# Kernel optimization log

Hardware: AMD Instinct MI355X
Metric: run time of the kernel (lower is better)

## Reference

```python
import jax, jax.numpy as jnp
import numpy as np

DIM = 1024
HEADS = 16
HEAD_DIM = DIM // HEADS
EXPANSION = 4
HIDDEN = int(DIM * EXPANSION * 2 / 3)  # 2730, per FFN code
LS_INIT = 1e-5
EPS = 1e-6


def setup_inputs() -> dict:
    key = jax.random.key(0)
    ks = jax.random.split(key, 16)
    s = lambda fan_in: 1.0 / np.sqrt(fan_in)
    return {
        "x": jax.random.normal(ks[0], (4, 1024, DIM), dtype=jnp.float32),
        "mask": jnp.ones((4, 1, 1, 1024), dtype=bool),
        "ln1_g": jnp.ones((DIM,), jnp.float32),
        "ln1_b": jnp.zeros((DIM,), jnp.float32),
        "qkv_w": jax.random.normal(ks[1], (DIM, 3 * DIM), jnp.float32) * s(DIM),
        "qkv_b": jnp.zeros((3 * DIM,), jnp.float32),
        "inter": jax.random.normal(ks[2], (HEADS, HEAD_DIM, HEAD_DIM), jnp.float32) * s(HEAD_DIM),
        "pl_w": jax.random.normal(ks[3], (HEADS, HEADS), jnp.float32) * s(HEADS),
        "pl_b": jnp.zeros((HEADS,), jnp.float32),
        "pw_w": jax.random.normal(ks[4], (HEADS, HEADS), jnp.float32) * s(HEADS),
        "pw_b": jnp.zeros((HEADS,), jnp.float32),
        "proj_w": jax.random.normal(ks[5], (DIM, DIM), jnp.float32) * s(DIM),
        "proj_b": jnp.zeros((DIM,), jnp.float32),
        "gamma1": jnp.full((DIM,), LS_INIT, jnp.float32),
        "ln2_g": jnp.ones((DIM,), jnp.float32),
        "ln2_b": jnp.zeros((DIM,), jnp.float32),
        "w_wide": jax.random.normal(ks[6], (DIM, HIDDEN), jnp.float32) * s(DIM),
        "w_gate": jax.random.normal(ks[7], (DIM, HIDDEN), jnp.float32) * s(DIM),
        "w_out": jax.random.normal(ks[8], (HIDDEN, DIM), jnp.float32) * s(HIDDEN),
        "gamma2": jnp.full((DIM,), LS_INIT, jnp.float32),
    }


def _layernorm(x, g, b):
    mu = jnp.mean(x, axis=-1, keepdims=True)
    var = jnp.mean(jnp.square(x - mu), axis=-1, keepdims=True)
    return (x - mu) * jax.lax.rsqrt(var + EPS) * g + b


def _forward(x, mask, ln1_g, ln1_b, qkv_w, qkv_b, inter, pl_w, pl_b, pw_w, pw_b,
             proj_w, proj_b, gamma1, ln2_g, ln2_b, w_wide, w_gate, w_out, gamma2):
    B, N, C = x.shape
    h = _layernorm(x, ln1_g, ln1_b)
    # talking-head attention with interaction matrix
    qkv = (h @ qkv_w + qkv_b).reshape(B, N, 3, HEADS, HEAD_DIM)
    qkv = jnp.transpose(qkv, (2, 0, 3, 1, 4))  # [3,B,H,N,hd]
    scale = jnp.asarray(HEAD_DIM ** -0.5, qkv.dtype)
    q, k, v = qkv[0] * scale, qkv[1], qkv[2]
    # attn[b,h,n,d] = q[b,h,n,i] * inter[h,i,j] * k[b,h,d,j]
    attn = jnp.einsum("bhni,hij,bhdj->bhnd", q, inter, k)
    # pre-softmax head mixing (proj_l), bias on head axis
    attn = jnp.einsum("bhnd,hg->bgnd", attn, pl_w) + pl_b[None, :, None, None]
    # keras Softmax with mask: add -1e9 to masked positions, softmax over last axis
    adder = (1.0 - mask.astype(attn.dtype)) * -1e9
    attn = jax.nn.softmax(attn + adder, axis=-1)
    # post-softmax head mixing (proj_w)
    attn = jnp.einsum("bhnd,hg->bgnd", attn, pw_w) + pw_b[None, :, None, None]
    o = jnp.einsum("bhnd,bhdc->bhnc", attn, v)  # [B,H,N,hd]
    o = jnp.transpose(o, (0, 2, 1, 3)).reshape(B, N, C)
    o = o @ proj_w + proj_b
    x1 = x + o * gamma1  # layerscale, stoch-depth identity at inference
    # SwiGLU-style FFN: relu(x W_wide) * (x W_gate) W_out
    h2 = _layernorm(x1, ln2_g, ln2_b)
    ff = (jax.nn.relu(h2 @ w_wide) * (h2 @ w_gate)) @ w_out
    return x1 + ff * gamma2


def reference(x, mask, ln1_g, ln1_b, qkv_w, qkv_b, inter, pl_w, pl_b, pw_w, pw_b,
              proj_w, proj_b, gamma1, ln2_g, ln2_b, w_wide, w_gate, w_out, gamma2):
    return _forward(x, mask, ln1_g, ln1_b, qkv_w, qkv_b, inter, pl_w, pl_b, pw_w,
                    pw_b, proj_w, proj_b, gamma1, ln2_g, ln2_b, w_wide, w_gate,
                    w_out, gamma2)
```

## Files before the change

kernel.cpp:

```cpp
#include <hip/hip_runtime.h>

using u16 = unsigned short;
using i64 = long long;
typedef u16   u16x4 __attribute__((ext_vector_type(4)));
typedef u16   u16x8 __attribute__((ext_vector_type(8)));
typedef short s16x4 __attribute__((ext_vector_type(4)));
typedef short s16x8 __attribute__((ext_vector_type(8)));
typedef float f32x4 __attribute__((ext_vector_type(4)));

__device__ __forceinline__ u16 f2bf(float f) {
    union { float f; unsigned u; } v; v.f = f;
    unsigned r = v.u + 0x7FFFu + ((v.u >> 16) & 1u);
    return (u16)(r >> 16);
}
__device__ __forceinline__ float bf2f(u16 a) {
    union { unsigned u; float f; } v; v.u = ((unsigned)a) << 16;
    return v.f;
}
__device__ __forceinline__ u16 f2bf_trunc(float f) {
    union { float f; unsigned u; } v; v.f = f;
    return (u16)(v.u >> 16);
}

#if defined(__has_builtin) && __has_builtin(__builtin_amdgcn_mfma_f32_16x16x16bf16_1k)
#define MFMA16(A, B, C) __builtin_amdgcn_mfma_f32_16x16x16bf16_1k(A, B, C, 0, 0, 0)
#else
static __device__ __forceinline__ f32x4 mfma16_asm(s16x4 a, s16x4 b, f32x4 c) {
    f32x4 d;
    asm volatile("v_mfma_f32_16x16x16_bf16 %0, %1, %2, %3\n\ts_nop 7\n\ts_nop 7"
                 : "=v"(d) : "v"(a), "v"(b), "v"(c));
    return d;
}
#define MFMA16(A, B, C) mfma16_asm(A, B, C)
#endif

static constexpr size_t O_H     = 0;
static constexpr size_t O_WALLT = 8388608;
static constexpr size_t O_BALL  = 14680064;
static constexpr size_t O_QI    = 14692352;
static constexpr size_t O_K     = 23080960;
static constexpr size_t O_VT    = 31469568;
static constexpr size_t O_PROJT = 39858176;
static constexpr size_t O_X1    = 41955328;
static constexpr size_t O_WGT   = 58732544;
static constexpr size_t O_WOUTT = 70266880;
static constexpr size_t O_S     = 75901952;
static constexpr size_t O_TBUF  = O_S + 46137344;

__global__ __launch_bounds__(256)
void ln_k(const float* __restrict__ x, const float* __restrict__ g,
          const float* __restrict__ b, u16* __restrict__ out) {
    int row = blockIdx.x, tid = threadIdx.x;
    const float4* xr = (const float4*)(x + (i64)row * 1024);
    float4 v = xr[tid];
    float s = v.x + v.y + v.z + v.w;
    float q = v.x * v.x + v.y * v.y + v.z * v.z + v.w * v.w;
    #pragma unroll
    for (int off = 32; off >= 1; off >>= 1) {
        s += __shfl_xor(s, off, 64);
        q += __shfl_xor(q, off, 64);
    }
    __shared__ float ps[8];
    int wv = tid >> 6, ln = tid & 63;
    if (ln == 0) { ps[wv] = s; ps[4 + wv] = q; }
    __syncthreads();
    s = ps[0] + ps[1] + ps[2] + ps[3];
    q = ps[4] + ps[5] + ps[6] + ps[7];
    float mu = s * (1.f / 1024.f);
    float var = q * (1.f / 1024.f) - mu * mu;
    float rs = rsqrtf(var + 1e-6f);
    float4 gv = ((const float4*)g)[tid];
    float4 bv = ((const float4*)b)[tid];
    u16x4 o;
    o[0] = f2bf((v.x - mu) * rs * gv.x + bv.x);
    o[1] = f2bf((v.y - mu) * rs * gv.y + bv.y);
    o[2] = f2bf((v.z - mu) * rs * gv.z + bv.z);
    o[3] = f2bf((v.w - mu) * rs * gv.w + bv.w);
    *(u16x4*)(out + (i64)row * 1024 + tid * 4) = o;
}

__global__ __launch_bounds__(256)
void transpose_cvt(const float* __restrict__ in, int ld_in, int Rin, int Cin,
                   u16* __restrict__ out, int Rout, int Cout, int rmul, int rbase) {
    __shared__ float tile[32][33];
    int tx = threadIdx.x, ty = threadIdx.y;
    int i0 = blockIdx.x * 32;
    int j0 = blockIdx.y * 32;
    #pragma unroll
    for (int r = 0; r < 4; r++) {
        int j = j0 + ty + r * 8, i = i0 + tx;
        tile[ty + r * 8][tx] = (j < Rin && i < Cin) ? in[(i64)j * ld_in + i] : 0.f;
    }
    __syncthreads();
    #pragma unroll
    for (int r = 0; r < 4; r++) {
        int i = i0 + ty + r * 8, j = j0 + tx;
        if (i < Rout && j < Cout)
            out[((i64)i * rmul + rbase) * Cout + j] = f2bf(tile[tx][ty + r * 8]);
    }
}

__global__ __launch_bounds__(256)
void fold_q(const float* __restrict__ qkv_w, const float* __restrict__ inter,
            u16* __restrict__ WallT) {
    __shared__ float ih[64 * 64];
    int h = blockIdx.x, i0 = blockIdx.y * 128, tid = threadIdx.x;
    for (int idx = tid; idx < 4096; idx += 256) ih[idx] = inter[h * 4096 + idx];
    __syncthreads();
    int i = i0 + (tid & 127);
    int jh = tid >> 7;
    const float* wr = qkv_w + (i64)i * 3072 + h * 64;
    float wreg[64];
    #pragma unroll
    for (int m = 0; m < 64; m++) wreg[m] = wr[m];
    for (int jj = 0; jj < 32; jj++) {
        int j = jh * 32 + jj;
        float s = 0.f;
        #pragma unroll
        for (int m = 0; m < 64; m++) s += wreg[m] * ih[m * 64 + j];
        WallT[(i64)(h * 64 + j) * 1024 + i] = f2bf(0.125f * s);
    }
}

__global__ void bias_fold(const float* __restrict__ qkv_b,
                          const float* __restrict__ inter, float* __restrict__ b_all) {
    int c = blockIdx.x * 256 + threadIdx.x;
    if (c >= 3072) return;
    if (c >= 1024) { b_all[c] = qkv_b[c]; return; }
    int h = c >> 6, j = c & 63;
    float s = 0.f;
    for (int m = 0; m < 64; m++) s += qkv_b[h * 64 + m] * inter[(h * 64 + m) * 64 + j];
    b_all[c] = 0.125f * s;
}

enum { EPI_BF16 = 0, EPI_QKV = 1, EPI_PV = 2, EPI_PROJ = 3, EPI_OUT = 4, EPI_FFN1 = 5 };

struct EpiP {
    void* p0; void* p1; void* p2;
    const float* f0; const float* f1; const float* f2;
    int ldc; i64 strideCb;
};

template<int BM, int BN, int EPI>
__global__ __launch_bounds__(256)
void gemm_nt(const u16* __restrict__ A, const u16* __restrict__ Bt,
             int lda, int ldb, int K, i64 sAb, i64 sBb, EpiP ep) {
    constexpr int WM = BM / 2, WN = BN / 2;
    constexpr int MR = WM / 16, NR = WN / 16;
    constexpr int ACH = (BM * 4) / 256, BCH = (BN * 4) / 256;
    __shared__ u16 As[BM * 40];
    __shared__ u16 Bs[BN * 40];
    const int tid = threadIdx.x;
    const int wave = tid >> 6, lane = tid & 63;
    const int wm = wave >> 1, wn = wave & 1;
    const int frow = lane & 15, kgrp = lane >> 4;
    const int tileM = blockIdx.x * BM, tileN = blockIdx.y * BN;
    const int z = blockIdx.z;
    const u16* Ab = A + (i64)z * sAb + (i64)tileM * lda;
    const u16* Bb = Bt + (i64)z * sBb + (i64)tileN * ldb;

    f32x4 acc[MR][NR];
    #pragma unroll
    for (int m = 0; m < MR; m++)
        #pragma unroll
        for (int n = 0; n < NR; n++) {
            acc[m][n][0] = 0.f; acc[m][n][1] = 0.f; acc[m][n][2] = 0.f; acc[m][n][3] = 0.f;
        }

    for (int k0 = 0; k0 < K; k0 += 32) {
        u16x8 av[ACH], bv[BCH];
        #pragma unroll
        for (int i = 0; i < ACH; i++) {
            int c = tid + i * 256;
            av[i] = *(const u16x8*)(Ab + (i64)(c >> 2) * lda + (k0 + (c & 3) * 8));
        }
        #pragma unroll
        for (int i = 0; i < BCH; i++) {
            int c = tid + i * 256;
            bv[i] = *(const u16x8*)(Bb + (i64)(c >> 2) * ldb + (k0 + (c & 3) * 8));
        }
        __syncthreads();
        #pragma unroll
        for (int i = 0; i < ACH; i++) {
            int c = tid + i * 256;
            *(u16x8*)&As[(c >> 2) * 40 + (c & 3) * 8] = av[i];
        }
        #pragma unroll
        for (int i = 0; i < BCH; i++) {
            int c = tid + i * 256;
            *(u16x8*)&Bs[(c >> 2) * 40 + (c & 3) * 8] = bv[i];
        }
        __syncthreads();
        s16x8 af[MR], bfr[NR];
        #pragma unroll
        for (int m = 0; m < MR; m++)
            af[m] = *(const s16x8*)&As[(wm * WM + m * 16 + frow) * 40 + kgrp * 8];
        #pragma unroll
        for (int n = 0; n < NR; n++)
            bfr[n] = *(const s16x8*)&Bs[(wn * WN + n * 16 + frow) * 40 + kgrp * 8];
        #pragma unroll
        for (int m = 0; m < MR; m++)
            #pragma unroll
            for (int n = 0; n < NR; n++)
                acc[m][n] = __builtin_amdgcn_mfma_f32_16x16x32_bf16(af[m], bfr[n], acc[m][n], 0, 0, 0);
    }

    #pragma unroll
    for (int m = 0; m < MR; m++) {
        int row0 = tileM + wm * WM + m * 16 + kgrp * 4;
        #pragma unroll
        for (int n = 0; n < NR; n++) {
            int col = tileN + wn * WN + n * 16 + frow;
            f32x4 v = acc[m][n];
            if constexpr (EPI == EPI_BF16) {
                u16* C = (u16*)ep.p0;
                i64 base = (i64)z * ep.strideCb;
                #pragma unroll
                for (int r = 0; r < 4; r++)
                    C[base + (i64)(row0 + r) * ep.ldc + col] = f2bf(v[r]);
            } else if constexpr (EPI == EPI_QKV) {
                float bias = ep.f0[col];
                int part = col >> 10, hc = col & 1023;
                int hh = hc >> 6, cc = hc & 63;
                u16* qi = (u16*)ep.p0; u16* kk = (u16*)ep.p1; u16* vt = (u16*)ep.p2;
                #pragma unroll
                for (int r = 0; r < 4; r++) {
                    int grow = row0 + r;
                    int b = grow >> 10, nn = grow & 1023;
                    u16 val = f2bf(v[r] + bias);
                    i64 bh = (i64)(b * 16 + hh);
                    if (part == 0)      qi[(bh * 1024 + nn) * 64 + cc] = val;
                    else if (part == 1) kk[(bh * 1024 + nn) * 64 + cc] = val;
                    else                vt[(bh * 64 + cc) * 1024 + nn] = val;
                }
            } else if constexpr (EPI == EPI_PV) {
                u16* ob = (u16*)ep.p0;
                int b = z >> 4, hh = z & 15;
                #pragma unroll
                for (int r = 0; r < 4; r++)
                    ob[((i64)(b * 1024 + row0 + r)) * 1024 + hh * 64 + col] = f2bf(v[r]);
            } else if constexpr (EPI == EPI_PROJ) {
                float* x1 = (float*)ep.p0;
                float pb = ep.f1[col], g1 = ep.f2[col];
                #pragma unroll
                for (int r = 0; r < 4; r++) {
                    i64 idx = (i64)(row0 + r) * 1024 + col;
                    x1[idx] = ep.f0[idx] + (v[r] + pb) * g1;
                }
            } else if constexpr (EPI == EPI_FFN1) {
                u16* t = (u16*)ep.p0;
                #pragma unroll
                for (int r = 0; r < 4; r++) {
                    float other = __shfl_xor(v[r], 1, 64);
                    if (!(lane & 1)) {
                        float w = v[r] > 0.f ? v[r] : 0.f;
                        t[(i64)(row0 + r) * 2752 + (col >> 1)] = f2bf(w * other);
                    }
                }
            } else {
                float* o = (float*)ep.p0;
                float g2 = ep.f1[col];
                #pragma unroll
                for (int r = 0; r < 4; r++) {
                    i64 idx = (i64)(row0 + r) * 1024 + col;
                    o[idx] = ep.f0[idx] + v[r] * g2;
                }
            }
        }
    }
}

__global__ __launch_bounds__(256)
void mix_softmax3(u16* __restrict__ S, const float* __restrict__ plwg,
                  const float* __restrict__ pwwg, const float* __restrict__ pwbg) {
    __shared__ u16 outb[16][1032];
    __shared__ float red[4][16];
    const int tid = threadIdx.x;
    const int wv = tid >> 6, l = tid & 63;
    const int grp = l >> 4, li = l & 15;
    const int b = blockIdx.y, n = blockIdx.x;
    u16* Sp = S + (i64)b * 16777216 + (i64)n * 1024;
    const int d0 = wv * 256;
    const float RCPLN2 = 1.4426950408889634f;

    s16x4 aPre;
    #pragma unroll
    for (int e = 0; e < 4; e++)
        aPre[e] = (short)f2bf(plwg[(grp * 4 + e) * 16 + li] * RCPLN2);

    f32x4 zero; zero[0] = 0.f; zero[1] = 0.f; zero[2] = 0.f; zero[3] = 0.f;

    f32x4 a[16];
    #pragma unroll
    for (int t = 0; t < 16; t++) {
        s16x4 bfr;
        #pragma unroll
        for (int e = 0; e < 4; e++)
            bfr[e] = (short)Sp[(i64)(grp * 4 + e) * 1048576 + (d0 + t * 16 + li)];
        a[t] = MFMA16(aPre, bfr, zero);
    }

    float mx[4];
    #pragma unroll
    for (int r = 0; r < 4; r++) {
        float m = a[0][r];
        #pragma unroll
        for (int t = 1; t < 16; t++) m = fmaxf(m, a[t][r]);
        #pragma unroll
        for (int off = 1; off < 16; off <<= 1) m = fmaxf(m, __shfl_xor(m, off, 64));
        mx[r] = m;
    }
    if (li == 0) {
        #pragma unroll
        for (int r = 0; r < 4; r++) red[wv][grp * 4 + r] = mx[r];
    }
    __syncthreads();
    #pragma unroll
    for (int r = 0; r < 4; r++) {
        int g = grp * 4 + r;
        mx[r] = fmaxf(fmaxf(red[0][g], red[1][g]), fmaxf(red[2][g], red[3][g]));
    }
    __syncthreads();

    #pragma unroll
    for (int t = 0; t < 16; t++) {
        #pragma unroll
        for (int r = 0; r < 4; r++) a[t][r] = exp2f(a[t][r] - mx[r]);
    }
    float sm[4];
    #pragma unroll
    for (int r = 0; r < 4; r++) {
        float s = a[0][r];
        #pragma unroll
        for (int t = 1; t < 16; t++) s += a[t][r];
        #pragma unroll
        for (int off = 1; off < 16; off <<= 1) s += __shfl_xor(s, off, 64);
        sm[r] = s;
    }
    if (li == 0) {
        #pragma unroll
        for (int r = 0; r < 4; r++) red[wv][grp * 4 + r] = sm[r];
    }
    __syncthreads();
    float inv[4];
    #pragma unroll
    for (int r = 0; r < 4; r++) {
        int g = grp * 4 + r;
        inv[r] = 1.f / ((red[0][g] + red[1][g]) + (red[2][g] + red[3][g]));
    }

    s16x4 pk[16];
    #pragma unroll
    for (int t = 0; t < 16; t++) {
        #pragma unroll
        for (int e = 0; e < 4; e++) pk[t][e] = (short)f2bf_trunc(a[t][e]);
    }

    s16x4 aPost;
    #pragma unroll
    for (int e = 0; e < 4; e++)
        aPost[e] = (short)f2bf(pwwg[(grp * 4 + e) * 16 + li] * inv[e]);
    f32x4 cinit;
    #pragma unroll
    for (int r = 0; r < 4; r++) cinit[r] = pwbg[grp * 4 + r];

    #pragma unroll
    for (int t = 0; t < 16; t++) {
        f32x4 o = MFMA16(aPost, pk[t], cinit);
        #pragma unroll
        for (int r = 0; r < 4; r++)
            outb[grp * 4 + r][d0 + t * 16 + li] = f2bf_trunc(o[r]);
    }
    __syncthreads();

    #pragma unroll
    for (int p = 0; p < 16; p++) {
        u16x4 v = *(const u16x4*)&outb[p][tid * 4];
        *(u16x4*)(Sp + (i64)p * 1048576 + tid * 4) = v;
    }
}

extern "C" void kernel_launch(void* const* d_in, const int* in_sizes, int n_in,
                              void* d_out, int out_size, void* d_ws, size_t ws_size,
                              hipStream_t stream) {
    (void)in_sizes; (void)n_in; (void)out_size; (void)ws_size;
    const float* x      = (const float*)d_in[0];
    const float* ln1_g  = (const float*)d_in[2];
    const float* ln1_b  = (const float*)d_in[3];
    const float* qkv_w  = (const float*)d_in[4];
    const float* qkv_b  = (const float*)d_in[5];
    const float* inter  = (const float*)d_in[6];
    const float* pl_w   = (const float*)d_in[7];
    const float* pw_w   = (const float*)d_in[9];
    const float* pw_b   = (const float*)d_in[10];
    const float* proj_w = (const float*)d_in[11];
    const float* proj_b = (const float*)d_in[12];
    const float* gamma1 = (const float*)d_in[13];
    const float* ln2_g  = (const float*)d_in[14];
    const float* ln2_b  = (const float*)d_in[15];
    const float* w_wide = (const float*)d_in[16];
    const float* w_gate = (const float*)d_in[17];
    const float* w_out  = (const float*)d_in[18];
    const float* gamma2 = (const float*)d_in[19];
    float* out = (float*)d_out;
    char* ws = (char*)d_ws;

    u16*   h     = (u16*)(ws + O_H);
    u16*   WallT = (u16*)(ws + O_WALLT);
    float* b_all = (float*)(ws + O_BALL);
    u16*   qi    = (u16*)(ws + O_QI);
    u16*   kb    = (u16*)(ws + O_K);
    u16*   vt    = (u16*)(ws + O_VT);
    u16*   projt = (u16*)(ws + O_PROJT);
    float* x1    = (float*)(ws + O_X1);
    u16*   wgt   = (u16*)(ws + O_WGT);
    u16*   woutt = (u16*)(ws + O_WOUTT);
    u16*   S     = (u16*)(ws + O_S);
    u16*   tbuf  = (u16*)(ws + O_TBUF);
    u16*   obuf  = qi;
    u16*   h2    = h;

    dim3 tb(32, 8);
    fold_q<<<dim3(16, 8), 256, 0, stream>>>(qkv_w, inter, WallT);
    bias_fold<<<12, 256, 0, stream>>>(qkv_b, inter, b_all);
    transpose_cvt<<<dim3(64, 32), tb, 0, stream>>>(qkv_w + 1024, 3072, 1024, 2048,
                                                   WallT + (i64)1024 * 1024, 2048, 1024, 1, 0);
    transpose_cvt<<<dim3(32, 32), tb, 0, stream>>>(proj_w, 1024, 1024, 1024, projt, 1024, 1024, 1, 0);
    transpose_cvt<<<dim3(86, 32), tb, 0, stream>>>(w_wide, 2730, 1024, 2730, wgt, 2752, 1024, 2, 0);
    transpose_cvt<<<dim3(86, 32), tb, 0, stream>>>(w_gate, 2730, 1024, 2730, wgt, 2752, 1024, 2, 1);
    transpose_cvt<<<dim3(32, 86), tb, 0, stream>>>(w_out, 1024, 2730, 1024, woutt, 1024, 2752, 1, 0);

    ln_k<<<4096, 256, 0, stream>>>(x, ln1_g, ln1_b, h);

    EpiP e_qkv = {}; e_qkv.p0 = qi; e_qkv.p1 = kb; e_qkv.p2 = vt; e_qkv.f0 = b_all;
    gemm_nt<128, 128, EPI_QKV><<<dim3(32, 24, 1), 256, 0, stream>>>(
        h, WallT, 1024, 1024, 1024, 0, 0, e_qkv);

    EpiP e_s = {}; e_s.p0 = S; e_s.ldc = 1024; e_s.strideCb = 1048576;
    gemm_nt<128, 128, EPI_BF16><<<dim3(8, 8, 64), 256, 0, stream>>>(
        qi, kb, 64, 64, 64, 65536, 65536, e_s);

    mix_softmax3<<<dim3(1024, 4), 256, 0, stream>>>(S, pl_w, pw_w, pw_b);

    EpiP e_pv = {}; e_pv.p0 = obuf;
    gemm_nt<128, 64, EPI_PV><<<dim3(8, 1, 64), 256, 0, stream>>>(
        S, vt, 1024, 1024, 1024, 1048576, 65536, e_pv);

    EpiP e_pr = {}; e_pr.p0 = x1; e_pr.f0 = x; e_pr.f1 = proj_b; e_pr.f2 = gamma1;
    gemm_nt<128, 128, EPI_PROJ><<<dim3(32, 8, 1), 256, 0, stream>>>(
        obuf, projt, 1024, 1024, 1024, 0, 0, e_pr);

    ln_k<<<4096, 256, 0, stream>>>(x1, ln2_g, ln2_b, h2);

    EpiP e_f1 = {}; e_f1.p0 = tbuf;
    gemm_nt<128, 128, EPI_FFN1><<<dim3(32, 43, 1), 256, 0, stream>>>(
        h2, wgt, 1024, 1024, 1024, 0, 0, e_f1);

    EpiP e_f2 = {}; e_f2.p0 = out; e_f2.f0 = x1; e_f2.f1 = gamma2;
    gemm_nt<128, 128, EPI_OUT><<<dim3(32, 8, 1), 256, 0, stream>>>(
        tbuf, woutt, 2752, 2752, 2752, 0, 0, e_f2);
}
```

Baseline: 525.1 us.

## Stream GEMM tiles into LDS with direct global loads and swizzled layout

The GEMM mainloop now copies A/B tiles straight from global memory into shared memory with global_load_lds, instead of staging them through registers. The LDS layout changes from a padded stride of 40 to a packed stride of 32 with an XOR swizzle on the 16-byte chunk index to avoid bank conflicts. The wide/gate weight interleave is changed from per-row to per-16-row blocks, so the FFN1 epilogue pairs adjacent accumulator fragments directly rather than using a lane shuffle. The goal is lower register pressure and lower copy-instruction overhead in the mainloop. The loop remains single-buffered, with two barriers per K step and no prefetch overlap.

After: 523.4 us. No clear change (-0.3%).

```diff
diff --git a/kernel.cpp b/kernel.cpp
--- a/kernel.cpp
+++ b/kernel.cpp
@@ -21,6 +21,10 @@
     union { float f; unsigned u; } v; v.f = f;
     return (u16)(v.u >> 16);
 }
+
+#define GLOAD16(g, l) \
+    __builtin_amdgcn_global_load_lds((const __attribute__((address_space(1))) void*)(g), \
+                                     (__attribute__((address_space(3))) void*)(l), 16, 0, 0)
 
 #if defined(__has_builtin) && __has_builtin(__builtin_amdgcn_mfma_f32_16x16x16bf16_1k)
 #define MFMA16(A, B, C) __builtin_amdgcn_mfma_f32_16x16x16bf16_1k(A, B, C, 0, 0, 0)
@@ -95,8 +99,10 @@
     #pragma unroll
     for (int r = 0; r < 4; r++) {
         int i = i0 + ty + r * 8, j = j0 + tx;
-        if (i < Rout && j < Cout)
-            out[((i64)i * rmul + rbase) * Cout + j] = f2bf(tile[tx][ty + r * 8]);
+        if (i < Rout && j < Cout) {
+            int orow = (rmul == 2) ? (((i >> 4) * 2 + rbase) * 16 + (i & 15)) : i;
+            out[(i64)orow * Cout + j] = f2bf(tile[tx][ty + r * 8]);
+        }
     }
 }
 
@@ -147,9 +153,8 @@
              int lda, int ldb, int K, i64 sAb, i64 sBb, EpiP ep) {
     constexpr int WM = BM / 2, WN = BN / 2;
     constexpr int MR = WM / 16, NR = WN / 16;
-    constexpr int ACH = (BM * 4) / 256, BCH = (BN * 4) / 256;
-    __shared__ u16 As[BM * 40];
-    __shared__ u16 Bs[BN * 40];
+    constexpr int ACH = BM / 16, CH = (BM + BN) / 16, NCH = CH / 4;
+    __shared__ u16 smem[(BM + BN) * 32];
     const int tid = threadIdx.x;
     const int wave = tid >> 6, lane = tid & 63;
     const int wm = wave >> 1, wn = wave & 1;
@@ -159,6 +164,21 @@
     const u16* Ab = A + (i64)z * sAb + (i64)tileM * lda;
     const u16* Bb = Bt + (i64)z * sBb + (i64)tileN * ldb;
 
+    const int rl = lane >> 2;
+    const int qsrc = (lane & 3) ^ ((lane >> 3) & 3);
+    const u16* gsrc[NCH];
+    const u16* lbase[NCH];
+    #pragma unroll
+    for (int i = 0; i < NCH; i++) {
+        int c = wave + i * 4;
+        gsrc[i] = (c < ACH) ? (Ab + (i64)(c * 16 + rl) * lda + qsrc * 8)
+                            : (Bb + (i64)((c - ACH) * 16 + rl) * ldb + qsrc * 8);
+        lbase[i] = smem + c * 512;
+    }
+    const int qrd = kgrp ^ ((frow >> 1) & 3);
+    const int aoff = (wm * WM + frow) * 32 + qrd * 8;
+    const int boff = (BM + wn * WN + frow) * 32 + qrd * 8;
+
     f32x4 acc[MR][NR];
     #pragma unroll
     for (int m = 0; m < MR; m++)
@@ -168,36 +188,18 @@
         }
 
     for (int k0 = 0; k0 < K; k0 += 32) {
-        u16x8 av[ACH], bv[BCH];
-        #pragma unroll
-        for (int i = 0; i < ACH; i++) {
-            int c = tid + i * 256;
-            av[i] = *(const u16x8*)(Ab + (i64)(c >> 2) * lda + (k0 + (c & 3) * 8));
-        }
-        #pragma unroll
-        for (int i = 0; i < BCH; i++) {
-            int c = tid + i * 256;
-            bv[i] = *(const u16x8*)(Bb + (i64)(c >> 2) * ldb + (k0 + (c & 3) * 8));
-        }
         __syncthreads();
         #pragma unroll
-        for (int i = 0; i < ACH; i++) {
-            int c = tid + i * 256;
-            *(u16x8*)&As[(c >> 2) * 40 + (c & 3) * 8] = av[i];
-        }
-        #pragma unroll
-        for (int i = 0; i < BCH; i++) {
-            int c = tid + i * 256;
-            *(u16x8*)&Bs[(c >> 2) * 40 + (c & 3) * 8] = bv[i];
-        }
+        for (int i = 0; i < NCH; i++)
+            GLOAD16(gsrc[i] + k0, lbase[i]);
         __syncthreads();
         s16x8 af[MR], bfr[NR];
         #pragma unroll
         for (int m = 0; m < MR; m++)
-            af[m] = *(const s16x8*)&As[(wm * WM + m * 16 + frow) * 40 + kgrp * 8];
+            af[m] = *(const s16x8*)&smem[aoff + m * 512];
         #pragma unroll
         for (int n = 0; n < NR; n++)
-            bfr[n] = *(const s16x8*)&Bs[(wn * WN + n * 16 + frow) * 40 + kgrp * 8];
+            bfr[n] = *(const s16x8*)&smem[boff + n * 512];
         #pragma unroll
         for (int m = 0; m < MR; m++)
             #pragma unroll
@@ -248,13 +250,13 @@
                     x1[idx] = ep.f0[idx] + (v[r] + pb) * g1;
                 }
             } else if constexpr (EPI == EPI_FFN1) {
-                u16* t = (u16*)ep.p0;
-                #pragma unroll
-                for (int r = 0; r < 4; r++) {
-                    float other = __shfl_xor(v[r], 1, 64);
-                    if (!(lane & 1)) {
-                        float w = v[r] > 0.f ? v[r] : 0.f;
-                        t[(i64)(row0 + r) * 2752 + (col >> 1)] = f2bf(w * other);
+                if ((n & 1) == 0) {
+                    u16* t = (u16*)ep.p0;
+                    int hc = ((tileN + wn * WN + n * 16) >> 5) * 16 + frow;
+                    #pragma unroll
+                    for (int r = 0; r < 4; r++) {
+                        float w = fmaxf(v[r], 0.f);
+                        t[(i64)(row0 + r) * 2752 + hc] = f2bf(w * acc[m][n + 1][r]);
                     }
                 }
             } else {
```
